# Kernel optimization log

Hardware: AMD Instinct MI355X
Metric: run time of the kernel (lower is better)

The kernel has to match this reference:

```python
import jax, jax.numpy as jnp
import numpy as np
from jax.ops import segment_sum, segment_max

N_NODES = 10000
N_EDGES = 160000
N_GRAPHS = 32
IN_DIM = 128
HID = 256
HEADS = 4


def setup_inputs() -> dict:
    key = jax.random.key(0)
    ks = jax.random.split(key, 12)
    x = jax.random.normal(ks[0], (N_NODES, IN_DIM), dtype=jnp.float32)
    edge_index = jax.random.randint(ks[1], (2, N_EDGES), 0, N_NODES, dtype=jnp.int64)
    batch = jnp.sort(jax.random.randint(ks[2], (N_NODES,), 0, N_GRAPHS, dtype=jnp.int64))
    s = 0.05
    params = {
        "W1": jax.random.normal(ks[3], (IN_DIM, HID), dtype=jnp.float32) * s,
        "b1": jnp.zeros((HID,), dtype=jnp.float32),
        "W2": jax.random.normal(ks[4], (HID, HID), dtype=jnp.float32) * s,
        "b2": jnp.zeros((HID,), dtype=jnp.float32),
        "Wg": jax.random.normal(ks[5], (HID, HEADS * HID), dtype=jnp.float32) * s,
        "att_src": jax.random.normal(ks[6], (HEADS, HID), dtype=jnp.float32) * s,
        "att_dst": jax.random.normal(ks[7], (HEADS, HID), dtype=jnp.float32) * s,
        "bg": jnp.zeros((HID,), dtype=jnp.float32),
        "W_heads": jax.random.normal(ks[8], (HID, 4), dtype=jnp.float32) * s,
        "b_heads": jnp.zeros((4,), dtype=jnp.float32),
    }
    return {"x": x, "edge_index": edge_index, "batch": batch, **params}


def _add_self_loops(edge_index, n):
    loop = jnp.arange(n, dtype=edge_index.dtype)
    src = jnp.concatenate([edge_index[0], loop])
    dst = jnp.concatenate([edge_index[1], loop])
    return src, dst


def _gcn_conv(x, W, b, src, dst, n):
    # PyG GCNConv: add self-loops, symmetric normalization D^-1/2 A D^-1/2
    h = x @ W                                   # [N, out]
    deg = segment_sum(jnp.ones_like(src, dtype=h.dtype), dst, num_segments=n)
    dinv = jax.lax.rsqrt(jnp.maximum(deg, 1e-12))
    coef = dinv[src] * dinv[dst]                # [E+N]
    out = segment_sum(h[src] * coef[:, None], dst, num_segments=n)
    return out + b


def _gat_conv(x, Wg, att_src, att_dst, bg, src, dst, n):
    # PyG GATConv(heads=4, concat=False): mean over heads, leaky_relu slope 0.2
    h = (x @ Wg).reshape(n, HEADS, HID)         # [N, H, C]
    a_src = jnp.einsum('nhc,hc->nh', h, att_src)
    a_dst = jnp.einsum('nhc,hc->nh', h, att_dst)
    e = jax.nn.leaky_relu(a_src[src] + a_dst[dst], 0.2)   # [E+N, H]
    m = segment_max(e, dst, num_segments=n)
    e = jnp.exp(e - m[dst])
    z = segment_sum(e, dst, num_segments=n)
    alpha = e / (z[dst] + 1e-16)                # softmax over edges into each dst
    out = segment_sum(h[src] * alpha[:, :, None], dst, num_segments=n)  # [N, H, C]
    return out.mean(axis=1) + bg


def reference(x, edge_index, batch, W1, b1, W2, b2, Wg, att_src, att_dst, bg, W_heads, b_heads):
    n = x.shape[0]
    src, dst = _add_self_loops(edge_index, n)
    h1 = jax.nn.relu(_gcn_conv(x, W1, b1, src, dst, n))
    h2 = jax.nn.relu(_gcn_conv(h1, W2, b2, src, dst, n))
    h3 = jax.nn.relu(_gat_conv(h2, Wg, att_src, att_dst, bg, src, dst, n))
    # global_mean_pool
    ones = jnp.ones((n,), dtype=h3.dtype)
    cnt = segment_sum(ones, batch, num_segments=N_GRAPHS)
    pooled = segment_sum(h3, batch, num_segments=N_GRAPHS) / jnp.maximum(cnt, 1.0)[:, None]
    # four scalar heads stacked: cols = [energy_absorption, elastic_modulus, ballistic_limit, penetration_resistance]
    return pooled @ W_heads + b_heads           # [G, 4]
```

## Files before the change

### kernel.cpp

```cpp
#include <hip/hip_runtime.h>
#include <cmath>

#define IN_DIM 128
#define HID 256
#define NHEADS 4
#define NGRAPHS 32

typedef unsigned short u16;
typedef __attribute__((ext_vector_type(8))) short bfrag8;
typedef __attribute__((ext_vector_type(4))) float f32x4;

__device__ __forceinline__ u16 f2bf(float x) {
  unsigned u = __float_as_uint(x);
  unsigned r = (u + 0x7fffu + ((u >> 16) & 1u)) >> 16;
  return (u16)r;
}
__device__ __forceinline__ float bf2f(u16 v) {
  return __uint_as_float(((unsigned)v) << 16);
}

__global__ __launch_bounds__(256) void count_edges_k(const int* __restrict__ dst,
                                                     int* __restrict__ cnt, int E) {
  int i = blockIdx.x * 256 + threadIdx.x;
  if (i < E) atomicAdd(&cnt[dst[i]], 1);
}

__global__ __launch_bounds__(1024) void scan_k(const int* __restrict__ cnt,
                                               int* __restrict__ row_ptr,
                                               float* __restrict__ dinv, int n) {
  __shared__ int sdata[1024];
  __shared__ int s_carry;
  if (threadIdx.x == 0) s_carry = 0;
  __syncthreads();
  int nchunks = (n + 1023) >> 10;
  for (int c = 0; c < nchunks; c++) {
    int i = (c << 10) + threadIdx.x;
    int v = (i < n) ? cnt[i] : 0;
    sdata[threadIdx.x] = v;
    __syncthreads();
    for (int off = 1; off < 1024; off <<= 1) {
      int t = (threadIdx.x >= off) ? sdata[threadIdx.x - off] : 0;
      __syncthreads();
      sdata[threadIdx.x] += t;
      __syncthreads();
    }
    int excl = sdata[threadIdx.x] - v;
    if (i < n) {
      row_ptr[i] = s_carry + excl;
      dinv[i] = rsqrtf((float)(v + 1));
    }
    __syncthreads();
    if (threadIdx.x == 0) s_carry += sdata[1023];
    __syncthreads();
  }
  if (threadIdx.x == 0) row_ptr[n] = s_carry;
}

__global__ __launch_bounds__(256) void fill_csr_k(const int* __restrict__ src,
                                                  const int* __restrict__ dst,
                                                  const int* __restrict__ row_ptr,
                                                  int* __restrict__ cursor,
                                                  int* __restrict__ csr_src, int E) {
  int i = blockIdx.x * 256 + threadIdx.x;
  if (i < E) {
    int d = dst[i];
    int p = atomicAdd(&cursor[d], 1);
    csr_src[row_ptr[d] + p] = src[i];
  }
}

__global__ __launch_bounds__(256) void pack_a_k(const float* __restrict__ A,
                                                u16* __restrict__ Ap,
                                                int K, int KT, int nfrag) {
  int wid = blockIdx.x * 4 + (threadIdx.x >> 6);
  int lane = threadIdx.x & 63;
  if (wid >= nfrag * KT) return;
  int fm = wid / KT, kt = wid - fm * KT;
  int m = fm * 16 + (lane & 15);
  int kb = kt * 32 + (lane >> 4) * 8;
  const float* src = A + (size_t)m * K + kb;
  float4 v0 = *(const float4*)src;
  float4 v1 = *(const float4*)(src + 4);
  float vv[8] = {v0.x, v0.y, v0.z, v0.w, v1.x, v1.y, v1.z, v1.w};
  u16 hi[8], lo[8];
  #pragma unroll
  for (int j = 0; j < 8; j++) {
    u16 h = f2bf(vv[j]);
    hi[j] = h;
    lo[j] = f2bf(vv[j] - bf2f(h));
  }
  u16* dst = Ap + ((size_t)fm * KT + kt) * 1024 + lane * 8;
  *(ushort4*)(dst)       = make_ushort4(hi[0], hi[1], hi[2], hi[3]);
  *(ushort4*)(dst + 4)   = make_ushort4(hi[4], hi[5], hi[6], hi[7]);
  *(ushort4*)(dst + 512) = make_ushort4(lo[0], lo[1], lo[2], lo[3]);
  *(ushort4*)(dst + 516) = make_ushort4(lo[4], lo[5], lo[6], lo[7]);
}

__global__ __launch_bounds__(256) void pack_b_k(const float* __restrict__ B,
                                                u16* __restrict__ Bp,
                                                int N, int KT, int nfrag) {
  int wid = blockIdx.x * 4 + (threadIdx.x >> 6);
  int lane = threadIdx.x & 63;
  if (wid >= nfrag * KT) return;
  int fn = wid / KT, kt = wid - fn * KT;
  int n = fn * 16 + (lane & 15);
  int kb = kt * 32 + (lane >> 4) * 8;
  float vv[8];
  #pragma unroll
  for (int j = 0; j < 8; j++) vv[j] = B[(size_t)(kb + j) * N + n];
  u16 hi[8], lo[8];
  #pragma unroll
  for (int j = 0; j < 8; j++) {
    u16 h = f2bf(vv[j]);
    hi[j] = h;
    lo[j] = f2bf(vv[j] - bf2f(h));
  }
  u16* dst = Bp + ((size_t)fn * KT + kt) * 1024 + lane * 8;
  *(ushort4*)(dst)       = make_ushort4(hi[0], hi[1], hi[2], hi[3]);
  *(ushort4*)(dst + 4)   = make_ushort4(hi[4], hi[5], hi[6], hi[7]);
  *(ushort4*)(dst + 512) = make_ushort4(lo[0], lo[1], lo[2], lo[3]);
  *(ushort4*)(dst + 516) = make_ushort4(lo[4], lo[5], lo[6], lo[7]);
}

template <int KT, int OMODE, bool ALO>
__global__ __launch_bounds__(256) void mfma_gemm_k(const u16* __restrict__ Ap,
                                                   const u16* __restrict__ Bp,
                                                   u16* __restrict__ Cb,
                                                   int M, int Nn) {
  int tid = threadIdx.x;
  int w = tid >> 6, lane = tid & 63;
  int wm = w >> 1, wn = w & 1;
  int fm0 = blockIdx.y * 4 + wm * 2;
  int fn0 = blockIdx.x * 4 + wn * 2;
  f32x4 acc[2][2] = {};
  #pragma unroll
  for (int kt = 0; kt < KT; kt++) {
    bfrag8 a_hi[2], a_lo[2], b_hi[2], b_lo[2];
    #pragma unroll
    for (int f = 0; f < 2; f++) {
      const u16* pa = Ap + ((size_t)(fm0 + f) * KT + kt) * 1024 + lane * 8;
      a_hi[f] = *(const bfrag8*)pa;
      if constexpr (ALO) a_lo[f] = *(const bfrag8*)(pa + 512);
      const u16* pb = Bp + ((size_t)(fn0 + f) * KT + kt) * 1024 + lane * 8;
      b_hi[f] = *(const bfrag8*)pb;
      b_lo[f] = *(const bfrag8*)(pb + 512);
    }
    #pragma unroll
    for (int f = 0; f < 2; f++) {
      #pragma unroll
      for (int g = 0; g < 2; g++) {
        acc[f][g] = __builtin_amdgcn_mfma_f32_16x16x32_bf16(a_hi[f], b_hi[g], acc[f][g], 0, 0, 0);
        acc[f][g] = __builtin_amdgcn_mfma_f32_16x16x32_bf16(a_hi[f], b_lo[g], acc[f][g], 0, 0, 0);
        if constexpr (ALO)
          acc[f][g] = __builtin_amdgcn_mfma_f32_16x16x32_bf16(a_lo[f], b_hi[g], acc[f][g], 0, 0, 0);
      }
    }
  }
  int r0 = (lane >> 4) * 4;
  int cl = lane & 15;
  #pragma unroll
  for (int f = 0; f < 2; f++) {
    #pragma unroll
    for (int g = 0; g < 2; g++) {
      int col = (fn0 + g) * 16 + cl;
      #pragma unroll
      for (int r = 0; r < 4; r++) {
        int row = (fm0 + f) * 16 + r0 + r;
        if (row < M) {
          if constexpr (OMODE == 1) {
            int head = col >> 8, cc = col & 255;
            Cb[((size_t)head * Nn + row) * HID + cc] = f2bf(acc[f][g][r]);
          } else {
            Cb[(size_t)row * HID + col] = f2bf(acc[f][g][r]);
          }
        }
      }
    }
  }
}

template <bool LOGITS, bool PACK_LO>
__global__ __launch_bounds__(256) void gcn_agg_k(const u16* __restrict__ t,
                                                 const int* __restrict__ row_ptr,
                                                 const int* __restrict__ csr_src,
                                                 const float* __restrict__ dinv,
                                                 const float* __restrict__ bias,
                                                 u16* __restrict__ apack,
                                                 const float* __restrict__ w_s,
                                                 const float* __restrict__ w_d,
                                                 float* __restrict__ a_src,
                                                 float* __restrict__ a_dst) {
  int i = blockIdx.x;
  int tt = threadIdx.x;
  int q = tt >> 6, lane = tt & 63;
  int c4 = lane * 4;
  __shared__ float4 s_part[4][64];
  float di = dinv[i];
  int beg = row_ptr[i], end = row_ptr[i + 1];
  float4 acc = make_float4(0.f, 0.f, 0.f, 0.f);
  if (q == 0) {
    ushort4 u = *(const ushort4*)&t[(size_t)i * HID + c4];
    float w = di * di;
    acc.x = w * bf2f(u.x); acc.y = w * bf2f(u.y);
    acc.z = w * bf2f(u.z); acc.w = w * bf2f(u.w);
  }
  int e = beg + q;
  for (; e + 4 < end; e += 8) {
    int s0 = csr_src[e], s1 = csr_src[e + 4];
    float w0 = dinv[s0] * di, w1 = dinv[s1] * di;
    ushort4 u0 = *(const ushort4*)&t[(size_t)s0 * HID + c4];
    ushort4 u1 = *(const ushort4*)&t[(size_t)s1 * HID + c4];
    acc.x += w0 * bf2f(u0.x) + w1 * bf2f(u1.x);
    acc.y += w0 * bf2f(u0.y) + w1 * bf2f(u1.y);
    acc.z += w0 * bf2f(u0.z) + w1 * bf2f(u1.z);
    acc.w += w0 * bf2f(u0.w) + w1 * bf2f(u1.w);
  }
  if (e < end) {
    int s = csr_src[e];
    float w = dinv[s] * di;
    ushort4 u = *(const ushort4*)&t[(size_t)s * HID + c4];
    acc.x += w * bf2f(u.x); acc.y += w * bf2f(u.y);
    acc.z += w * bf2f(u.z); acc.w += w * bf2f(u.w);
  }
  s_part[q][lane] = acc;
  __syncthreads();
  int c = tt;
  const float* f = (const float*)s_part;
  float a = (f[c] + f[256 + c]) + (f[512 + c] + f[768 + c]);
  float v = fmaxf(a + bias[c], 0.f);
  {
    int fm = i >> 4, kt = c >> 5;
    int pl = (i & 15) + 16 * ((c >> 3) & 3);
    int j = c & 7;
    u16 h = f2bf(v);
    size_t base = ((size_t)fm * 8 + kt) * 1024 + pl * 8 + j;
    apack[base] = h;
    if constexpr (PACK_LO) apack[base + 512] = f2bf(v - bf2f(h));
  }
  if constexpr (LOGITS) {
    __shared__ float s_rs[4][NHEADS];
    __shared__ float s_rd[4][NHEADS];
    float4 wsv = *(const float4*)&w_s[c * NHEADS];
    float4 wdv = *(const float4*)&w_d[c * NHEADS];
    float ps[NHEADS] = {v * wsv.x, v * wsv.y, v * wsv.z, v * wsv.w};
    float pd[NHEADS] = {v * wdv.x, v * wdv.y, v * wdv.z, v * wdv.w};
    #pragma unroll
    for (int off = 32; off; off >>= 1) {
      #pragma unroll
      for (int h = 0; h < NHEADS; h++) {
        ps[h] += __shfl_xor(ps[h], off);
        pd[h] += __shfl_xor(pd[h], off);
      }
    }
    int wv = q;
    if (lane == 0) {
      #pragma unroll
      for (int h = 0; h < NHEADS; h++) { s_rs[wv][h] = ps[h]; s_rd[wv][h] = pd[h]; }
    }
    __syncthreads();
    if (tt < NHEADS)
      a_src[i * NHEADS + tt] = s_rs[0][tt] + s_rs[1][tt] + s_rs[2][tt] + s_rs[3][tt];
    else if (tt < 2 * NHEADS) {
      int h = tt - NHEADS;
      a_dst[i * NHEADS + h] = s_rd[0][h] + s_rd[1][h] + s_rd[2][h] + s_rd[3][h];
    }
  }
}

__global__ __launch_bounds__(256) void watt_k(const float* __restrict__ Wg,
                                              const float* __restrict__ att_src,
                                              const float* __restrict__ att_dst,
                                              float* __restrict__ w_s,
                                              float* __restrict__ w_d) {
  int k = blockIdx.x;
  int c = threadIdx.x;
  int wv = c >> 6, ln = c & 63;
  __shared__ float red_s[4][NHEADS];
  __shared__ float red_d[4][NHEADS];
  #pragma unroll
  for (int h = 0; h < NHEADS; h++) {
    float w = Wg[(size_t)k * (NHEADS * HID) + h * HID + c];
    float vs = w * att_src[h * HID + c];
    float vd = w * att_dst[h * HID + c];
    #pragma unroll
    for (int off = 32; off; off >>= 1) {
      vs += __shfl_xor(vs, off);
      vd += __shfl_xor(vd, off);
    }
    if (ln == 0) { red_s[wv][h] = vs; red_d[wv][h] = vd; }
  }
  __syncthreads();
  if (c < NHEADS) {
    w_s[k * NHEADS + c] = red_s[0][c] + red_s[1][c] + red_s[2][c] + red_s[3][c];
    w_d[k * NHEADS + c] = red_d[0][c] + red_d[1][c] + red_d[2][c] + red_d[3][c];
  }
}

__device__ __forceinline__ float lrelu02(float x) { return x > 0.f ? x : 0.2f * x; }

__global__ __launch_bounds__(256) void gat_agg_k(const u16* __restrict__ hgT,
                                                 const int* __restrict__ row_ptr,
                                                 const int* __restrict__ csr_src,
                                                 const float* __restrict__ a_src,
                                                 const float* __restrict__ a_dst,
                                                 const float* __restrict__ bg,
                                                 float* __restrict__ out, int Nn) {
  int i = blockIdx.x;
  int t = threadIdx.x;
  int hw = t >> 6, lane = t & 63;
  __shared__ int s_src[NHEADS][64];
  __shared__ float s_al[NHEADS][64];
  __shared__ float s_acc[NHEADS][64][4];
  int beg = row_ptr[i], end = row_ptr[i + 1];
  int deg = end - beg;
  float adh = a_dst[i * NHEADS + hw];
  const u16* slab = hgT + (size_t)hw * Nn * HID;
  int c4 = lane * 4;
  float a0 = 0.f, a1 = 0.f, a2 = 0.f, a3 = 0.f;

  if (deg <= 63) {
    int s = (lane < deg) ? csr_src[beg + lane] : i;
    bool valid = (lane <= deg);
    float logit = valid ? lrelu02(a_src[s * NHEADS + hw] + adh) : -INFINITY;
    float m = logit;
    #pragma unroll
    for (int off = 32; off; off >>= 1) m = fmaxf(m, __shfl_xor(m, off));
    float ex = valid ? expf(logit - m) : 0.f;
    float z = ex;
    #pragma unroll
    for (int off = 32; off; off >>= 1) z += __shfl_xor(z, off);
    float al = ex / (z + 1e-16f);
    s_src[hw][lane] = s;
    s_al[hw][lane] = al;
    int nk = deg + 1;
    int e = 0;
    for (; e + 3 < nk; e += 4) {
      int s0 = s_src[hw][e + 0], s1 = s_src[hw][e + 1];
      int s2 = s_src[hw][e + 2], s3 = s_src[hw][e + 3];
      float w0 = s_al[hw][e + 0], w1 = s_al[hw][e + 1];
      float w2 = s_al[hw][e + 2], w3 = s_al[hw][e + 3];
      ushort4 v0 = *(const ushort4*)&slab[(size_t)s0 * HID + c4];
      ushort4 v1 = *(const ushort4*)&slab[(size_t)s1 * HID + c4];
      ushort4 v2 = *(const ushort4*)&slab[(size_t)s2 * HID + c4];
      ushort4 v3 = *(const ushort4*)&slab[(size_t)s3 * HID + c4];
      a0 += w0 * bf2f(v0.x) + w1 * bf2f(v1.x) + w2 * bf2f(v2.x) + w3 * bf2f(v3.x);
      a1 += w0 * bf2f(v0.y) + w1 * bf2f(v1.y) + w2 * bf2f(v2.y) + w3 * bf2f(v3.y);
      a2 += w0 * bf2f(v0.z) + w1 * bf2f(v1.z) + w2 * bf2f(v2.z) + w3 * bf2f(v3.z);
      a3 += w0 * bf2f(v0.w) + w1 * bf2f(v1.w) + w2 * bf2f(v2.w) + w3 * bf2f(v3.w);
    }
    for (; e < nk; e++) {
      int se = s_src[hw][e];
      float ae = s_al[hw][e];
      ushort4 v = *(const ushort4*)&slab[(size_t)se * HID + c4];
      a0 += ae * bf2f(v.x); a1 += ae * bf2f(v.y);
      a2 += ae * bf2f(v.z); a3 += ae * bf2f(v.w);
    }
  } else {
    float lself = lrelu02(a_src[i * NHEADS + hw] + adh);
    float m = lself;
    for (int e = beg + lane; e < end; e += 64)
      m = fmaxf(m, lrelu02(a_src[csr_src[e] * NHEADS + hw] + adh));
    #pragma unroll
    for (int off = 32; off; off >>= 1) m = fmaxf(m, __shfl_xor(m, off));
    float z = (lane == 0) ? expf(lself - m) : 0.f;
    for (int e = beg + lane; e < end; e += 64)
      z += expf(lrelu02(a_src[csr_src[e] * NHEADS + hw] + adh) - m);
    #pragma unroll
    for (int off = 32; off; off >>= 1) z += __shfl_xor(z, off);
    float iz = 1.f / (z + 1e-16f);
    {
      float ae = expf(lself - m) * iz;
      ushort4 v = *(const ushort4*)&slab[(size_t)i * HID + c4];
      a0 += ae * bf2f(v.x); a1 += ae * bf2f(v.y);
      a2 += ae * bf2f(v.z); a3 += ae * bf2f(v.w);
    }
    for (int base = beg; base < end; base += 64) {
      int mc = min(64, end - base);
      int s = (lane < mc) ? csr_src[base + lane] : 0;
      float al = (lane < mc)
                     ? expf(lrelu02(a_src[s * NHEADS + hw] + adh) - m) * iz
                     : 0.f;
      s_src[hw][lane] = s;
      s_al[hw][lane] = al;
      for (int e = 0; e < mc; e++) {
        int se = s_src[hw][e];
        float ae = s_al[hw][e];
        ushort4 v = *(const ushort4*)&slab[(size_t)se * HID + c4];
        a0 += ae * bf2f(v.x); a1 += ae * bf2f(v.y);
        a2 += ae * bf2f(v.z); a3 += ae * bf2f(v.w);
      }
    }
  }
  s_acc[hw][lane][0] = a0;
  s_acc[hw][lane][1] = a1;
  s_acc[hw][lane][2] = a2;
  s_acc[hw][lane][3] = a3;
  __syncthreads();
  int c = t;
  const float* f = (const float*)s_acc;
  float a = (f[c] + f[256 + c]) + (f[512 + c] + f[768 + c]);
  out[(size_t)i * HID + c] = fmaxf(a * 0.25f + bg[c], 0.f);
}

#define POOL_CHUNK 50
__global__ __launch_bounds__(256) void pool_acc_k(const float* __restrict__ h3,
                                                  const int* __restrict__ batch,
                                                  float* __restrict__ pooled,
                                                  float* __restrict__ gcnt, int N) {
  int c = threadIdx.x;
  int i0 = blockIdx.x * POOL_CHUNK;
  int i1 = min(i0 + POOL_CHUNK, N);
  if (i0 >= N) return;
  float acc = 0.f;
  int cur = batch[i0];
  int cnt_local = 0;
  for (int i = i0; i < i1; i++) {
    int g = batch[i];
    if (g != cur) {
      atomicAdd(&pooled[cur * HID + c], acc);
      if (c == 0) atomicAdd(&gcnt[cur], (float)cnt_local);
      acc = 0.f;
      cnt_local = 0;
      cur = g;
    }
    acc += h3[(size_t)i * HID + c];
    cnt_local++;
  }
  atomicAdd(&pooled[cur * HID + c], acc);
  if (c == 0) atomicAdd(&gcnt[cur], (float)cnt_local);
}

__global__ __launch_bounds__(128) void head_k(const float* __restrict__ pooled,
                                              const float* __restrict__ gcnt,
                                              const float* __restrict__ W_heads,
                                              const float* __restrict__ b_heads,
                                              float* __restrict__ out) {
  int tid = threadIdx.x;
  if (tid >= NGRAPHS * 4) return;
  int g = tid >> 2, k = tid & 3;
  float invc = 1.f / fmaxf(gcnt[g], 1.f);
  float acc = 0.f;
  for (int c = 0; c < HID; c++) acc += pooled[g * HID + c] * W_heads[c * 4 + k];
  out[g * 4 + k] = acc * invc + b_heads[k];
}

extern "C" void kernel_launch(void* const* d_in, const int* in_sizes, int n_in,
                              void* d_out, int out_size, void* d_ws, size_t ws_size,
                              hipStream_t stream) {
  const float* x = (const float*)d_in[0];
  const int* ei = (const int*)d_in[1];
  const int* batch = (const int*)d_in[2];
  const float* W1 = (const float*)d_in[3];
  const float* b1 = (const float*)d_in[4];
  const float* W2 = (const float*)d_in[5];
  const float* b2 = (const float*)d_in[6];
  const float* Wg = (const float*)d_in[7];
  const float* att_src = (const float*)d_in[8];
  const float* att_dst = (const float*)d_in[9];
  const float* bg = (const float*)d_in[10];
  const float* W_heads = (const float*)d_in[11];
  const float* b_heads = (const float*)d_in[12];
  float* out = (float*)d_out;

  const int N = in_sizes[0] / IN_DIM;
  const int E = in_sizes[1] / 2;
  const int* src = ei;
  const int* dst = ei + E;

  const int NFM = N / 16;
  const int NFMP = ((N + 63) / 64) * 4;

  char* ws = (char*)d_ws;
  size_t off = 0;
  auto take = [&](size_t bytes) -> char* {
    char* p = ws + off;
    off = (off + bytes + 255) & ~(size_t)255;
    return p;
  };
  int* cnt      = (int*)take((size_t)N * 4);
  int* row_ptr  = (int*)take((size_t)(N + 1) * 4);
  int* cursor   = (int*)take((size_t)N * 4);
  int* csr_src  = (int*)take((size_t)E * 4);
  float* dinv   = (float*)take((size_t)N * 4);
  float* a_srcv = (float*)take((size_t)N * NHEADS * 4);
  float* a_dstv = (float*)take((size_t)N * NHEADS * 4);
  float* w_s    = (float*)take((size_t)HID * NHEADS * 4);
  float* w_d    = (float*)take((size_t)HID * NHEADS * 4);
  float* pooled = (float*)take((size_t)NGRAPHS * HID * 4 + NGRAPHS * 4);
  float* gcnt   = pooled + NGRAPHS * HID;
  u16*   tb     = (u16*)take((size_t)N * HID * 2);
  float* h3     = (float*)take((size_t)N * HID * 4);
  u16*   hgT    = (u16*)take((size_t)N * NHEADS * HID * 2);
  u16*   xp     = (u16*)take((size_t)NFMP * 4 * 1024 * 2);
  u16*   h1p    = (u16*)take((size_t)NFMP * 8 * 1024 * 2);
  u16*   h2p    = (u16*)take((size_t)NFMP * 8 * 1024 * 2);
  u16*   w1p    = (u16*)take((size_t)16 * 4 * 1024 * 2);
  u16*   w2p    = (u16*)take((size_t)16 * 8 * 1024 * 2);
  u16*   wgp    = (u16*)take((size_t)64 * 8 * 1024 * 2);

  hipMemsetAsync(cnt, 0, (size_t)N * 4, stream);
  hipMemsetAsync(cursor, 0, (size_t)N * 4, stream);
  hipMemsetAsync(pooled, 0, (size_t)NGRAPHS * HID * 4 + NGRAPHS * 4, stream);

  int eb = (E + 255) / 256;
  count_edges_k<<<eb, 256, 0, stream>>>(dst, cnt, E);
  scan_k<<<1, 1024, 0, stream>>>(cnt, row_ptr, dinv, N);
  fill_csr_k<<<eb, 256, 0, stream>>>(src, dst, row_ptr, cursor, csr_src, E);
  watt_k<<<HID, 256, 0, stream>>>(Wg, att_src, att_dst, w_s, w_d);

  pack_a_k<<<(NFM * 4 + 3) / 4, 256, 0, stream>>>(x, xp, IN_DIM, 4, NFM);
  pack_b_k<<<(16 * 4 + 3) / 4, 256, 0, stream>>>(W1, w1p, HID, 4, 16);
  pack_b_k<<<(16 * 8 + 3) / 4, 256, 0, stream>>>(W2, w2p, HID, 8, 16);
  pack_b_k<<<(64 * 8 + 3) / 4, 256, 0, stream>>>(Wg, wgp, NHEADS * HID, 8, 64);

  int mg64 = (N + 63) / 64;
  mfma_gemm_k<4, 0, true><<<dim3(4, mg64), 256, 0, stream>>>(xp, w1p, tb, N, N);
  gcn_agg_k<false, true><<<N, 256, 0, stream>>>(tb, row_ptr, csr_src, dinv, b1,
                                                h1p, nullptr, nullptr, nullptr, nullptr);
  mfma_gemm_k<8, 0, true><<<dim3(4, mg64), 256, 0, stream>>>(h1p, w2p, tb, N, N);
  gcn_agg_k<true, false><<<N, 256, 0, stream>>>(tb, row_ptr, csr_src, dinv, b2,
                                                h2p, w_s, w_d, a_srcv, a_dstv);
  mfma_gemm_k<8, 1, false><<<dim3(16, mg64), 256, 0, stream>>>(h2p, wgp, hgT, N, N);
  gat_agg_k<<<N, 256, 0, stream>>>(hgT, row_ptr, csr_src, a_srcv, a_dstv, bg, h3, N);
  int pb = (N + POOL_CHUNK - 1) / POOL_CHUNK;
  pool_acc_k<<<pb, 256, 0, stream>>>(h3, batch, pooled, gcnt, N);
  head_k<<<1, 128, 0, stream>>>(pooled, gcnt, W_heads, b_heads, out);
}
```

Before: 232.5 us.

## Map one wavefront per node in aggregations, fuse prep kernels, shuffle-based scan

The GCN and GAT aggregation kernels now assign one wavefront per destination node instead of a 256-thread block. Each lane handles a contiguous slice of channels, and float4 attention logits are reduced with cross-lane shuffles instead of shared-memory reductions. The GAT GEMM writes a node-major layout so each node's head rows are contiguous. Packing and attention-weight precompute are fused into one prep launch, the scan uses wave shuffles, and the three memsets collapse into one. This cuts launches, barriers and shared-memory traffic, but each wave now does more serial edge work per node.

```diff
diff --git a/kernel.cpp b/kernel.cpp
--- a/kernel.cpp
+++ b/kernel.cpp
@@ -18,6 +18,9 @@
 __device__ __forceinline__ float bf2f(u16 v) {
   return __uint_as_float(((unsigned)v) << 16);
 }
+__device__ __forceinline__ float lof(unsigned u) { return __uint_as_float(u << 16); }
+__device__ __forceinline__ float hif(unsigned u) { return __uint_as_float(u & 0xffff0000u); }
+__device__ __forceinline__ float lrelu02(float x) { return x > 0.f ? x : 0.2f * x; }
 
 __global__ __launch_bounds__(256) void count_edges_k(const int* __restrict__ dst,
                                                      int* __restrict__ cnt, int E) {
@@ -28,32 +31,44 @@
 __global__ __launch_bounds__(1024) void scan_k(const int* __restrict__ cnt,
                                                int* __restrict__ row_ptr,
                                                float* __restrict__ dinv, int n) {
-  __shared__ int sdata[1024];
-  __shared__ int s_carry;
-  if (threadIdx.x == 0) s_carry = 0;
-  __syncthreads();
-  int nchunks = (n + 1023) >> 10;
-  for (int c = 0; c < nchunks; c++) {
-    int i = (c << 10) + threadIdx.x;
+  __shared__ int s_w[16];
+  __shared__ int s_tot;
+  int tid = threadIdx.x;
+  int wv = tid >> 6, lane = tid & 63;
+  int carry = 0;
+  int nch = (n + 1023) >> 10;
+  for (int c = 0; c < nch; c++) {
+    int i = (c << 10) + tid;
     int v = (i < n) ? cnt[i] : 0;
-    sdata[threadIdx.x] = v;
+    int incl = v;
+    #pragma unroll
+    for (int off = 1; off < 64; off <<= 1) {
+      int t = __shfl_up(incl, off);
+      if (lane >= off) incl += t;
+    }
+    if (lane == 63) s_w[wv] = incl;
     __syncthreads();
-    for (int off = 1; off < 1024; off <<= 1) {
-      int t = (threadIdx.x >= off) ? sdata[threadIdx.x - off] : 0;
-      __syncthreads();
-      sdata[threadIdx.x] += t;
-      __syncthreads();
-    }
-    int excl = sdata[threadIdx.x] - v;
+    if (tid < 16) {
+      int sv = s_w[tid];
+      int si = sv;
+      #pragma unroll
+      for (int off = 1; off < 16; off <<= 1) {
+        int t = __shfl_up(si, off, 16);
+        if (tid >= off) si += t;
+      }
+      s_w[tid] = si - sv;
+      if (tid == 15) s_tot = si;
+    }
+    __syncthreads();
+    int excl = incl - v + s_w[wv] + carry;
     if (i < n) {
-      row_ptr[i] = s_carry + excl;
+      row_ptr[i] = excl;
       dinv[i] = rsqrtf((float)(v + 1));
     }
+    carry += s_tot;
     __syncthreads();
-    if (threadIdx.x == 0) s_carry += sdata[1023];
-    __syncthreads();
-  }
-  if (threadIdx.x == 0) row_ptr[n] = s_carry;
+  }
+  if (tid == 0) row_ptr[n] = carry;
 }
 
 __global__ __launch_bounds__(256) void fill_csr_k(const int* __restrict__ src,
@@ -69,12 +84,8 @@
   }
 }
 
-__global__ __launch_bounds__(256) void pack_a_k(const float* __restrict__ A,
-                                                u16* __restrict__ Ap,
-                                                int K, int KT, int nfrag) {
-  int wid = blockIdx.x * 4 + (threadIdx.x >> 6);
-  int lane = threadIdx.x & 63;
-  if (wid >= nfrag * KT) return;
+__device__ void pack_a_dev(const float* __restrict__ A, u16* __restrict__ Ap,
+                           int K, int KT, int wid, int lane) {
   int fm = wid / KT, kt = wid - fm * KT;
   int m = fm * 16 + (lane & 15);
   int kb = kt * 32 + (lane >> 4) * 8;
@@ -89,19 +100,15 @@
     hi[j] = h;
     lo[j] = f2bf(vv[j] - bf2f(h));
   }
-  u16* dst = Ap + ((size_t)fm * KT + kt) * 1024 + lane * 8;
-  *(ushort4*)(dst)       = make_ushort4(hi[0], hi[1], hi[2], hi[3]);
-  *(ushort4*)(dst + 4)   = make_ushort4(hi[4], hi[5], hi[6], hi[7]);
-  *(ushort4*)(dst + 512) = make_ushort4(lo[0], lo[1], lo[2], lo[3]);
-  *(ushort4*)(dst + 516) = make_ushort4(lo[4], lo[5], lo[6], lo[7]);
-}
-
-__global__ __launch_bounds__(256) void pack_b_k(const float* __restrict__ B,
-                                                u16* __restrict__ Bp,
-                                                int N, int KT, int nfrag) {
-  int wid = blockIdx.x * 4 + (threadIdx.x >> 6);
-  int lane = threadIdx.x & 63;
-  if (wid >= nfrag * KT) return;
+  u16* dstp = Ap + ((size_t)fm * KT + kt) * 1024 + lane * 8;
+  *(ushort4*)(dstp)       = make_ushort4(hi[0], hi[1], hi[2], hi[3]);
+  *(ushort4*)(dstp + 4)   = make_ushort4(hi[4], hi[5], hi[6], hi[7]);
+  *(ushort4*)(dstp + 512) = make_ushort4(lo[0], lo[1], lo[2], lo[3]);
+  *(ushort4*)(dstp + 516) = make_ushort4(lo[4], lo[5], lo[6], lo[7]);
+}
+
+__device__ void pack_b_dev(const float* __restrict__ B, u16* __restrict__ Bp,
+                           int N, int KT, int wid, int lane) {
   int fn = wid / KT, kt = wid - fn * KT;
   int n = fn * 16 + (lane & 15);
   int kb = kt * 32 + (lane >> 4) * 8;
@@ -115,18 +122,69 @@
     hi[j] = h;
     lo[j] = f2bf(vv[j] - bf2f(h));
   }
-  u16* dst = Bp + ((size_t)fn * KT + kt) * 1024 + lane * 8;
-  *(ushort4*)(dst)       = make_ushort4(hi[0], hi[1], hi[2], hi[3]);
-  *(ushort4*)(dst + 4)   = make_ushort4(hi[4], hi[5], hi[6], hi[7]);
-  *(ushort4*)(dst + 512) = make_ushort4(lo[0], lo[1], lo[2], lo[3]);
-  *(ushort4*)(dst + 516) = make_ushort4(lo[4], lo[5], lo[6], lo[7]);
-}
-
-template <int KT, int OMODE, bool ALO>
+  u16* dstp = Bp + ((size_t)fn * KT + kt) * 1024 + lane * 8;
+  *(ushort4*)(dstp)       = make_ushort4(hi[0], hi[1], hi[2], hi[3]);
+  *(ushort4*)(dstp + 4)   = make_ushort4(hi[4], hi[5], hi[6], hi[7]);
+  *(ushort4*)(dstp + 512) = make_ushort4(lo[0], lo[1], lo[2], lo[3]);
+  *(ushort4*)(dstp + 516) = make_ushort4(lo[4], lo[5], lo[6], lo[7]);
+}
+
+__global__ __launch_bounds__(256) void prep_k(const float* __restrict__ x,
+                                              const float* __restrict__ W1,
+                                              const float* __restrict__ W2,
+                                              const float* __restrict__ Wg,
+                                              const float* __restrict__ att_src,
+                                              const float* __restrict__ att_dst,
+                                              u16* __restrict__ xp,
+                                              u16* __restrict__ w1p,
+                                              u16* __restrict__ w2p,
+                                              u16* __restrict__ wgp,
+                                              float* __restrict__ w_s,
+                                              float* __restrict__ w_d, int NFM) {
+  __shared__ float red_s[4][NHEADS];
+  __shared__ float red_d[4][NHEADS];
+  int b = blockIdx.x;
+  int tid = threadIdx.x;
+  int lane = tid & 63;
+  int XB = NFM;
+  if (b < XB) {
+    int wid = b * 4 + (tid >> 6);
+    if (wid < NFM * 4) pack_a_dev(x, xp, IN_DIM, 4, wid, lane);
+  } else if (b < XB + 16) {
+    pack_b_dev(W1, w1p, HID, 4, (b - XB) * 4 + (tid >> 6), lane);
+  } else if (b < XB + 48) {
+    pack_b_dev(W2, w2p, HID, 8, (b - XB - 16) * 4 + (tid >> 6), lane);
+  } else if (b < XB + 176) {
+    pack_b_dev(Wg, wgp, NHEADS * HID, 8, (b - XB - 48) * 4 + (tid >> 6), lane);
+  } else {
+    int k = b - (XB + 176);
+    int c = tid, wvv = c >> 6, ln = c & 63;
+    #pragma unroll
+    for (int h = 0; h < NHEADS; h++) {
+      float w = Wg[(size_t)k * (NHEADS * HID) + h * HID + c];
+      float vs = w * att_src[h * HID + c];
+      float vd = w * att_dst[h * HID + c];
+      #pragma unroll
+      for (int off = 32; off; off >>= 1) {
+        vs += __shfl_xor(vs, off);
+        vd += __shfl_xor(vd, off);
+      }
+      if (ln == 0) { red_s[wvv][h] = vs; red_d[wvv][h] = vd; }
+    }
+    __syncthreads();
+    if (c < NHEADS)
+      w_s[k * NHEADS + c] = red_s[0][c] + red_s[1][c] + red_s[2][c] + red_s[3][c];
+    else if (c < 2 * NHEADS) {
+      int h = c - NHEADS;
+      w_d[k * NHEADS + h] = red_d[0][h] + red_d[1][h] + red_d[2][h] + red_d[3][h];
+    }
+  }
+}
+
+template <int KT, int LDC, bool ALO>
 __global__ __launch_bounds__(256) void mfma_gemm_k(const u16* __restrict__ Ap,
                                                    const u16* __restrict__ Bp,
-                                                   u16* __restrict__ Cb,
-                                                   int M, int Nn) {
+                                                   u16* __restrict__ Cb, int M) {
   int tid = threadIdx.x;
   int w = tid >> 6, lane = tid & 63;
   int wm = w >> 1, wn = w & 1;
@@ -166,14 +224,7 @@
       #pragma unroll
       for (int r = 0; r < 4; r++) {
         int row = (fm0 + f) * 16 + r0 + r;
-        if (row < M) {
-          if constexpr (OMODE == 1) {
-            int head = col >> 8, cc = col & 255;
-            Cb[((size_t)head * Nn + row) * HID + cc] = f2bf(acc[f][g][r]);
-          } else {
-            Cb[(size_t)row * HID + col] = f2bf(acc[f][g][r]);
-          }
-        }
+        if (row < M) Cb[(size_t)row * LDC + col] = f2bf(acc[f][g][r]);
       }
     }
   }
@@ -188,218 +239,235 @@
                                                  u16* __restrict__ apack,
                                                  const float* __restrict__ w_s,
                                                  const float* __restrict__ w_d,
-                                                 float* __restrict__ a_src,
-                                                 float* __restrict__ a_dst) {
-  int i = blockIdx.x;
-  int tt = threadIdx.x;
-  int q = tt >> 6, lane = tt & 63;
+                                                 float4* __restrict__ a_src4,
+                                                 float4* __restrict__ a_dst4, int N) {
+  int wv = threadIdx.x >> 6, lane = threadIdx.x & 63;
+  int i = blockIdx.x * 4 + wv;
+  if (i >= N) return;
+  float di = dinv[i];
   int c4 = lane * 4;
-  __shared__ float4 s_part[4][64];
-  float di = dinv[i];
   int beg = row_ptr[i], end = row_ptr[i + 1];
-  float4 acc = make_float4(0.f, 0.f, 0.f, 0.f);
-  if (q == 0) {
-    ushort4 u = *(const ushort4*)&t[(size_t)i * HID + c4];
+  float a0, a1, a2, a3;
+  {
+    uint2 u = *(const uint2*)&t[(size_t)i * HID + c4];
     float w = di * di;
-    acc.x = w * bf2f(u.x); acc.y = w * bf2f(u.y);
-    acc.z = w * bf2f(u.z); acc.w = w * bf2f(u.w);
-  }
-  int e = beg + q;
-  for (; e + 4 < end; e += 8) {
-    int s0 = csr_src[e], s1 = csr_src[e + 4];
+    a0 = w * lof(u.x); a1 = w * hif(u.x); a2 = w * lof(u.y); a3 = w * hif(u.y);
+  }
+  int e = beg;
+  for (; e + 3 < end; e += 4) {
+    int s0 = csr_src[e + 0], s1 = csr_src[e + 1];
+    int s2 = csr_src[e + 2], s3 = csr_src[e + 3];
     float w0 = dinv[s0] * di, w1 = dinv[s1] * di;
-    ushort4 u0 = *(const ushort4*)&t[(size_t)s0 * HID + c4];
-    ushort4 u1 = *(const ushort4*)&t[(size_t)s1 * HID + c4];
-    acc.x += w0 * bf2f(u0.x) + w1 * bf2f(u1.x);
-    acc.y += w0 * bf2f(u0.y) + w1 * bf2f(u1.y);
-    acc.z += w0 * bf2f(u0.z) + w1 * bf2f(u1.z);
-    acc.w += w0 * bf2f(u0.w) + w1 * bf2f(u1.w);
-  }
-  if (e < end) {
+    float w2 = dinv[s2] * di, w3 = dinv[s3] * di;
+    uint2 u0 = *(const uint2*)&t[(size_t)s0 * HID + c4];
+    uint2 u1 = *(const uint2*)&t[(size_t)s1 * HID + c4];
+    uint2 u2 = *(const uint2*)&t[(size_t)s2 * HID + c4];
+    uint2 u3 = *(const uint2*)&t[(size_t)s3 * HID + c4];
+    a0 += w0 * lof(u0.x) + w1 * lof(u1.x) + w2 * lof(u2.x) + w3 * lof(u3.x);
+    a1 += w0 * hif(u0.x) + w1 * hif(u1.x) + w2 * hif(u2.x) + w3 * hif(u3.x);
+    a2 += w0 * lof(u0.y) + w1 * lof(u1.y) + w2 * lof(u2.y) + w3 * lof(u3.y);
+    a3 += w0 * hif(u0.y) + w1 * hif(u1.y) + w2 * hif(u2.y) + w3 * hif(u3.y);
+  }
+  for (; e < end; e++) {
     int s = csr_src[e];
     float w = dinv[s] * di;
-    ushort4 u = *(const ushort4*)&t[(size_t)s * HID + c4];
-    acc.x += w * bf2f(u.x); acc.y += w * bf2f(u.y);
-    acc.z += w * bf2f(u.z); acc.w += w * bf2f(u.w);
-  }
-  s_part[q][lane] = acc;
-  __syncthreads();
-  int c = tt;
-  const float* f = (const float*)s_part;
-  float a = (f[c] + f[256 + c]) + (f[512 + c] + f[768 + c]);
-  float v = fmaxf(a + bias[c], 0.f);
+    uint2 u = *(const uint2*)&t[(size_t)s * HID + c4];
+    a0 += w * lof(u.x); a1 += w * hif(u.x); a2 += w * lof(u.y); a3 += w * hif(u.y);
+  }
+  float4 bv = *(const float4*)&bias[c4];
+  float v0 = fmaxf(a0 + bv.x, 0.f), v1 = fmaxf(a1 + bv.y, 0.f);
+  float v2 = fmaxf(a2 + bv.z, 0.f), v3 = fmaxf(a3 + bv.w, 0.f);
   {
-    int fm = i >> 4, kt = c >> 5;
-    int pl = (i & 15) + 16 * ((c >> 3) & 3);
-    int j = c & 7;
-    u16 h = f2bf(v);
-    size_t base = ((size_t)fm * 8 + kt) * 1024 + pl * 8 + j;
-    apack[base] = h;
-    if constexpr (PACK_LO) apack[base + 512] = f2bf(v - bf2f(h));
+    int fm = i >> 4, kt = c4 >> 5;
+    int pl = (i & 15) + 16 * ((c4 >> 3) & 3);
+    int j0 = c4 & 7;
+    size_t base = ((size_t)fm * 8 + kt) * 1024 + pl * 8 + j0;
+    u16 h0 = f2bf(v0), h1 = f2bf(v1), h2 = f2bf(v2), h3 = f2bf(v3);
+    *(ushort4*)&apack[base] = make_ushort4(h0, h1, h2, h3);
+    if constexpr (PACK_LO)
+      *(ushort4*)&apack[base + 512] =
+          make_ushort4(f2bf(v0 - bf2f(h0)), f2bf(v1 - bf2f(h1)),
+                       f2bf(v2 - bf2f(h2)), f2bf(v3 - bf2f(h3)));
   }
   if constexpr (LOGITS) {
-    __shared__ float s_rs[4][NHEADS];
-    __shared__ float s_rd[4][NHEADS];
-    float4 wsv = *(const float4*)&w_s[c * NHEADS];
-    float4 wdv = *(const float4*)&w_d[c * NHEADS];
-    float ps[NHEADS] = {v * wsv.x, v * wsv.y, v * wsv.z, v * wsv.w};
-    float pd[NHEADS] = {v * wdv.x, v * wdv.y, v * wdv.z, v * wdv.w};
+    const float4* ws4 = (const float4*)w_s;
+    const float4* wd4 = (const float4*)w_d;
+    float4 s0 = ws4[c4 + 0], s1 = ws4[c4 + 1], s2 = ws4[c4 + 2], s3 = ws4[c4 + 3];
+    float4 d0 = wd4[c4 + 0], d1 = wd4[c4 + 1], d2 = wd4[c4 + 2], d3 = wd4[c4 + 3];
+    float ps0 = v0 * s0.x + v1 * s1.x + v2 * s2.x + v3 * s3.x;
+    float ps1 = v0 * s0.y + v1 * s1.y + v2 * s2.y + v3 * s3.y;
+    float ps2 = v0 * s0.z + v1 * s1.z + v2 * s2.z + v3 * s3.z;
+    float ps3 = v0 * s0.w + v1 * s1.w + v2 * s2.w + v3 * s3.w;
+    float pd0 = v0 * d0.x + v1 * d1.x + v2 * d2.x + v3 * d3.x;
+    float pd1 = v0 * d0.y + v1 * d1.y + v2 * d2.y + v3 * d3.y;
+    float pd2 = v0 * d0.z + v1 * d1.z + v2 * d2.z + v3 * d3.z;
+    float pd3 = v0 * d0.w + v1 * d1.w + v2 * d2.w + v3 * d3.w;
     #pragma unroll
     for (int off = 32; off; off >>= 1) {
-      #pragma unroll
-      for (int h = 0; h < NHEADS; h++) {
-        ps[h] += __shfl_xor(ps[h], off);
-        pd[h] += __shfl_xor(pd[h], off);
-      }
-    }
-    int wv = q;
+      ps0 += __shfl_xor(ps0, off); ps1 += __shfl_xor(ps1, off);
+      ps2 += __shfl_xor(ps2, off); ps3 += __shfl_xor(ps3, off);
+      pd0 += __shfl_xor(pd0, off); pd1 += __shfl_xor(pd1, off);
+      pd2 += __shfl_xor(pd2, off); pd3 += __shfl_xor(pd3, off);
+    }
     if (lane == 0) {
-      #pragma unroll
-      for (int h = 0; h < NHEADS; h++) { s_rs[wv][h] = ps[h]; s_rd[wv][h] = pd[h]; }
-    }
-    __syncthreads();
-    if (tt < NHEADS)
-      a_src[i * NHEADS + tt] = s_rs[0][tt] + s_rs[1][tt] + s_rs[2][tt] + s_rs[3][tt];
-    else if (tt < 2 * NHEADS) {
-      int h = tt - NHEADS;
-      a_dst[i * NHEADS + h] = s_rd[0][h] + s_rd[1][h] + s_rd[2][h] + s_rd[3][h];
-    }
-  }
-}
-
-__global__ __launch_bounds__(256) void watt_k(const float* __restrict__ Wg,
-                                              const float* __restrict__ att_src,
-                                              const float* __restrict__ att_dst,
-                                              float* __restrict__ w_s,
-                                              float* __restrict__ w_d) {
-  int k = blockIdx.x;
-  int c = threadIdx.x;
-  int wv = c >> 6, ln = c & 63;
-  __shared__ float red_s[4][NHEADS];
-  __shared__ float red_d[4][NHEADS];
-  #pragma unroll
-  for (int h = 0; h < NHEADS; h++) {
-    float w = Wg[(size_t)k * (NHEADS * HID) + h * HID + c];
-    float vs = w * att_src[h * HID + c];
-    float vd = w * att_dst[h * HID + c];
-    #pragma unroll
-    for (int off = 32; off; off >>= 1) {
-      vs += __shfl_xor(vs, off);
-      vd += __shfl_xor(vd, off);
-    }
-    if (ln == 0) { red_s[wv][h] = vs; red_d[wv][h] = vd; }
-  }
-  __syncthreads();
-  if (c < NHEADS) {
-    w_s[k * NHEADS + c] = red_s[0][c] + red_s[1][c] + red_s[2][c] + red_s[3][c];
-    w_d[k * NHEADS + c] = red_d[0][c] + red_d[1][c] + red_d[2][c] + red_d[3][c];
-  }
-}
-
-__device__ __forceinline__ float lrelu02(float x) { return x > 0.f ? x : 0.2f * x; }
+      a_src4[i] = make_float4(ps0, ps1, ps2, ps3);
+      a_dst4[i] = make_float4(pd0, pd1, pd2, pd3);
+    }
+  }
+}
+
+#define ACC8(U, AW, O)                                         \
+  acc[O + 0] += (AW) * lof((U).x); acc[O + 1] += (AW) * hif((U).x); \
+  acc[O + 2] += (AW) * lof((U).y); acc[O + 3] += (AW) * hif((U).y); \
+  acc[O + 4] += (AW) * lof((U).z); acc[O + 5] += (AW) * hif((U).z); \
+  acc[O + 6] += (AW) * lof((U).w); acc[O + 7] += (AW) * hif((U).w);
 
 __global__ __launch_bounds__(256) void gat_agg_k(const u16* __restrict__ hgT,
                                                  const int* __restrict__ row_ptr,
                                                  const int* __restrict__ csr_src,
-                                                 const float* __restrict__ a_src,
-                                                 const float* __restrict__ a_dst,
+                                                 const float4* __restrict__ a_src4,
+                                                 const float4* __restrict__ a_dst4,
                                                  const float* __restrict__ bg,
-                                                 float* __restrict__ out, int Nn) {
-  int i = blockIdx.x;
-  int t = threadIdx.x;
-  int hw = t >> 6, lane = t & 63;
-  __shared__ int s_src[NHEADS][64];
-  __shared__ float s_al[NHEADS][64];
-  __shared__ float s_acc[NHEADS][64][4];
+                                                 float* __restrict__ out, int N) {
+  __shared__ int s_src[4][64];
+  __shared__ float s_al[4][NHEADS][65];
+  int wv = threadIdx.x >> 6, lane = threadIdx.x & 63;
+  int i = blockIdx.x * 4 + wv;
+  if (i >= N) return;
   int beg = row_ptr[i], end = row_ptr[i + 1];
   int deg = end - beg;
-  float adh = a_dst[i * NHEADS + hw];
-  const u16* slab = hgT + (size_t)hw * Nn * HID;
-  int c4 = lane * 4;
-  float a0 = 0.f, a1 = 0.f, a2 = 0.f, a3 = 0.f;
-
+  float4 ad = a_dst4[i];
+  int hw = lane >> 4;
+  float acc[16];
+  #pragma unroll
+  for (int j = 0; j < 16; j++) acc[j] = 0.f;
+  const u16* rowbase = hgT + (size_t)lane * 16;
+
+  int nk;
   if (deg <= 63) {
     int s = (lane < deg) ? csr_src[beg + lane] : i;
     bool valid = (lane <= deg);
-    float logit = valid ? lrelu02(a_src[s * NHEADS + hw] + adh) : -INFINITY;
-    float m = logit;
-    #pragma unroll
-    for (int off = 32; off; off >>= 1) m = fmaxf(m, __shfl_xor(m, off));
-    float ex = valid ? expf(logit - m) : 0.f;
-    float z = ex;
-    #pragma unroll
-    for (int off = 32; off; off >>= 1) z += __shfl_xor(z, off);
-    float al = ex / (z + 1e-16f);
-    s_src[hw][lane] = s;
-    s_al[hw][lane] = al;
-    int nk = deg + 1;
+    float4 as = a_src4[s];
+    float l0 = valid ? lrelu02(as.x + ad.x) : -INFINITY;
+    float l1 = valid ? lrelu02(as.y + ad.y) : -INFINITY;
+    float l2 = valid ? lrelu02(as.z + ad.z) : -INFINITY;
+    float l3 = valid ? lrelu02(as.w + ad.w) : -INFINITY;
+    float m0 = l0, m1 = l1, m2 = l2, m3 = l3;
+    #pragma unroll
+    for (int off = 32; off; off >>= 1) {
+      m0 = fmaxf(m0, __shfl_xor(m0, off)); m1 = fmaxf(m1, __shfl_xor(m1, off));
+      m2 = fmaxf(m2, __shfl_xor(m2, off)); m3 = fmaxf(m3, __shfl_xor(m3, off));
+    }
+    float e0 = valid ? expf(l0 - m0) : 0.f;
+    float e1 = valid ? expf(l1 - m1) : 0.f;
+    float e2 = valid ? expf(l2 - m2) : 0.f;
+    float e3 = valid ? expf(l3 - m3) : 0.f;
+    float z0 = e0, z1 = e1, z2 = e2, z3 = e3;
+    #pragma unroll
+    for (int off = 32; off; off >>= 1) {
+      z0 += __shfl_xor(z0, off); z1 += __shfl_xor(z1, off);
+      z2 += __shfl_xor(z2, off); z3 += __shfl_xor(z3, off);
+    }
+    s_src[wv][lane] = s;
+    s_al[wv][0][lane] = e0 / (z0 + 1e-16f);
+    s_al[wv][1][lane] = e1 / (z1 + 1e-16f);
+    s_al[wv][2][lane] = e2 / (z2 + 1e-16f);
+    s_al[wv][3][lane] = e3 / (z3 + 1e-16f);
+    nk = deg + 1;
     int e = 0;
-    for (; e + 3 < nk; e += 4) {
-      int s0 = s_src[hw][e + 0], s1 = s_src[hw][e + 1];
-      int s2 = s_src[hw][e + 2], s3 = s_src[hw][e + 3];
-      float w0 = s_al[hw][e + 0], w1 = s_al[hw][e + 1];
-      float w2 = s_al[hw][e + 2], w3 = s_al[hw][e + 3];
-      ushort4 v0 = *(const ushort4*)&slab[(size_t)s0 * HID + c4];
-      ushort4 v1 = *(const ushort4*)&slab[(size_t)s1 * HID + c4];
-      ushort4 v2 = *(const ushort4*)&slab[(size_t)s2 * HID + c4];
-      ushort4 v3 = *(const ushort4*)&slab[(size_t)s3 * HID + c4];
-      a0 += w0 * bf2f(v0.x) + w1 * bf2f(v1.x) + w2 * bf2f(v2.x) + w3 * bf2f(v3.x);
-      a1 += w0 * bf2f(v0.y) + w1 * bf2f(v1.y) + w2 * bf2f(v2.y) + w3 * bf2f(v3.y);
-      a2 += w0 * bf2f(v0.z) + w1 * bf2f(v1.z) + w2 * bf2f(v2.z) + w3 * bf2f(v3.z);
-      a3 += w0 * bf2f(v0.w) + w1 * bf2f(v1.w) + w2 * bf2f(v2.w) + w3 * bf2f(v3.w);
-    }
-    for (; e < nk; e++) {
-      int se = s_src[hw][e];
-      float ae = s_al[hw][e];
-      ushort4 v = *(const ushort4*)&slab[(size_t)se * HID + c4];
-      a0 += ae * bf2f(v.x); a1 += ae * bf2f(v.y);
-      a2 += ae * bf2f(v.z); a3 += ae * bf2f(v.w);
+    for (; e + 1 < nk; e += 2) {
+      int sa = s_src[wv][e], sb = s_src[wv][e + 1];
+      float awa = s_al[wv][hw][e], awb = s_al[wv][hw][e + 1];
+      const uint4* ra = (const uint4*)(rowbase + (size_t)sa * 1024);
+      const uint4* rb = (const uint4*)(rowbase + (size_t)sb * 1024);
+      uint4 ua0 = ra[0], ua1 = ra[1];
+      uint4 ub0 = rb[0], ub1 = rb[1];
+      ACC8(ua0, awa, 0); ACC8(ua1, awa, 8);
+      ACC8(ub0, awb, 0); ACC8(ub1, awb, 8);
+    }
+    if (e < nk) {
+      int sa = s_src[wv][e];
+      float awa = s_al[wv][hw][e];
+      const uint4* ra = (const uint4*)(rowbase + (size_t)sa * 1024);
+      uint4 ua0 = ra[0], ua1 = ra[1];
+      ACC8(ua0, awa, 0); ACC8(ua1, awa, 8);
     }
   } else {
-    float lself = lrelu02(a_src[i * NHEADS + hw] + adh);
-    float m = lself;
-    for (int e = beg + lane; e < end; e += 64)
-      m = fmaxf(m, lrelu02(a_src[csr_src[e] * NHEADS + hw] + adh));
-    #pragma unroll
-    for (int off = 32; off; off >>= 1) m = fmaxf(m, __shfl_xor(m, off));
-    float z = (lane == 0) ? expf(lself - m) : 0.f;
-    for (int e = beg + lane; e < end; e += 64)
-      z += expf(lrelu02(a_src[csr_src[e] * NHEADS + hw] + adh) - m);
-    #pragma unroll
-    for (int off = 32; off; off >>= 1) z += __shfl_xor(z, off);
-    float iz = 1.f / (z + 1e-16f);
+    float4 asi = a_src4[i];
+    float ls0 = lrelu02(asi.x + ad.x), ls1 = lrelu02(asi.y + ad.y);
+    float ls2 = lrelu02(asi.z + ad.z), ls3 = lrelu02(asi.w + ad.w);
+    float m0 = ls0, m1 = ls1, m2 = ls2, m3 = ls3;
+    for (int e = beg + lane; e < end; e += 64) {
+      float4 as = a_src4[csr_src[e]];
+      m0 = fmaxf(m0, lrelu02(as.x + ad.x)); m1 = fmaxf(m1, lrelu02(as.y + ad.y));
+      m2 = fmaxf(m2, lrelu02(as.z + ad.z)); m3 = fmaxf(m3, lrelu02(as.w + ad.w));
+    }
+    #pragma unroll
+    for (int off = 32; off; off >>= 1) {
+      m0 = fmaxf(m0, __shfl_xor(m0, off)); m1 = fmaxf(m1, __shfl_xor(m1, off));
+      m2 = fmaxf(m2, __shfl_xor(m2, off)); m3 = fmaxf(m3, __shfl_xor(m3, off));
+    }
+    float z0 = (lane == 0) ? expf(ls0 - m0) : 0.f;
+    float z1 = (lane == 0) ? expf(ls1 - m1) : 0.f;
+    float z2 = (lane == 0) ? expf(ls2 - m2) : 0.f;
+    float z3 = (lane == 0) ? expf(ls3 - m3) : 0.f;
+    for (int e = beg + lane; e < end; e += 64) {
+      float4 as = a_src4[csr_src[e]];
+      z0 += expf(lrelu02(as.x + ad.x) - m0); z1 += expf(lrelu02(as.y + ad.y) - m1);
+      z2 += expf(lrelu02(as.z + ad.z) - m2); z3 += expf(lrelu02(as.w + ad.w) - m3);
+    }
+    #pragma unroll
+    for (int off = 32; off; off >>= 1) {
+      z0 += __shfl_xor(z0, off); z1 += __shfl_xor(z1, off);
+      z2 += __shfl_xor(z2, off); z3 += __shfl_xor(z3, off);
+    }
+    float iz0 = 1.f / (z0 + 1e-16f), iz1 = 1.f / (z1 + 1e-16f);
+    float iz2 = 1.f / (z2 + 1e-16f), iz3 = 1.f / (z3 + 1e-16f);
     {
-      float ae = expf(lself - m) * iz;
-      ushort4 v = *(const ushort4*)&slab[(size_t)i * HID + c4];
-      a0 += ae * bf2f(v.x); a1 += ae * bf2f(v.y);
-      a2 += ae * bf2f(v.z); a3 += ae * bf2f(v.w);
+      float w0 = expf(ls0 - m0) * iz0, w1 = expf(ls1 - m1) * iz1;
+      float w2 = expf(ls2 - m2) * iz2, w3 = expf(ls3 - m3) * iz3;
+      float aw = hw == 0 ? w0 : hw == 1 ? w1 : hw == 2 ? w2 : w3;
+      const uint4* r = (const uint4*)(rowbase + (size_t)i * 1024);
+      uint4 u0 = r[0], u1 = r[1];
+      ACC8(u0, aw, 0); ACC8(u1, aw, 8);
     }
     for (int base = beg; base < end; base += 64) {
       int mc = min(64, end - base);
-      int s = (lane < mc) ? csr_src[base + lane] : 0;
-      float al = (lane < mc)
-                     ? expf(lrelu02(a_src[s * NHEADS + hw] + adh) - m) * iz
-                     : 0.f;
-      s_src[hw][lane] = s;
-      s_al[hw][lane] = al;
+      if (lane < mc) {
+        int s = csr_src[base + lane];
+        float4 as = a_src4[s];
+        s_src[wv][lane] = s;
+        s_al[wv][0][lane] = expf(lrelu02(as.x + ad.x) - m0) * iz0;
+        s_al[wv][1][lane] = expf(lrelu02(as.y + ad.y) - m1) * iz1;
+        s_al[wv][2][lane] = expf(lrelu02(as.z + ad.z) - m2) * iz2;
+        s_al[wv][3][lane] = expf(lrelu02(as.w + ad.w) - m3) * iz3;
+      }
       for (int e = 0; e < mc; e++) {
-        int se = s_src[hw][e];
-        float ae = s_al[hw][e];
-        ushort4 v = *(const ushort4*)&slab[(size_t)se * HID + c4];
-        a0 += ae * bf2f(v.x); a1 += ae * bf2f(v.y);
-        a2 += ae * bf2f(v.z); a3 += ae * bf2f(v.w);
+        int sa = s_src[wv][e];
+        float awa = s_al[wv][hw][e];
+        const uint4* ra = (const uint4*)(rowbase + (size_t)sa * 1024);
+        uint4 ua0 = ra[0], ua1 = ra[1];
+        ACC8(ua0, awa, 0); ACC8(ua1, awa, 8);
       }
     }
   }
-  s_acc[hw][lane][0] = a0;
-  s_acc[hw][lane][1] = a1;
-  s_acc[hw][lane][2] = a2;
-  s_acc[hw][lane][3] = a3;
-  __syncthreads();
-  int c = t;
-  const float* f = (const float*)s_acc;
-  float a = (f[c] + f[256 + c]) + (f[512 + c] + f[768 + c]);
-  out[(size_t)i * HID + c] = fmaxf(a * 0.25f + bg[c], 0.f);
+  #pragma unroll
+  for (int j = 0; j < 16; j++) {
+    acc[j] += __shfl_xor(acc[j], 16);
+    acc[j] += __shfl_xor(acc[j], 32);
+  }
+  if (lane < 16) {
+    int cb = lane * 16;
+    float o[16];
+    #pragma unroll
+    for (int j = 0; j < 16; j++)
+      o[j] = fmaxf(acc[j] * 0.25f + bg[cb + j], 0.f);
+    float* op = out + (size_t)i * HID + cb;
+    *(float4*)(op + 0)  = make_float4(o[0], o[1], o[2], o[3]);
+    *(float4*)(op + 4)  = make_float4(o[4], o[5], o[6], o[7]);
+    *(float4*)(op + 8)  = make_float4(o[8], o[9], o[10], o[11]);
+    *(float4*)(op + 12) = make_float4(o[12], o[13], o[14], o[15]);
+  }
 }
 
 #define POOL_CHUNK 50
@@ -478,16 +546,17 @@
     return p;
   };
   int* cnt      = (int*)take((size_t)N * 4);
+  int* cursor   = (int*)take((size_t)N * 4);
+  float* pooled = (float*)take((size_t)NGRAPHS * HID * 4 + NGRAPHS * 4);
+  float* gcnt   = pooled + NGRAPHS * HID;
+  size_t zero_span = off;
   int* row_ptr  = (int*)take((size_t)(N + 1) * 4);
-  int* cursor   = (int*)take((size_t)N * 4);
   int* csr_src  = (int*)take((size_t)E * 4);
   float* dinv   = (float*)take((size_t)N * 4);
-  float* a_srcv = (float*)take((size_t)N * NHEADS * 4);
-  float* a_dstv = (float*)take((size_t)N * NHEADS * 4);
+  float4* a_src4 = (float4*)take((size_t)N * 16);
+  float4* a_dst4 = (float4*)take((size_t)N * 16);
   float* w_s    = (float*)take((size_t)HID * NHEADS * 4);
   float* w_d    = (float*)take((size_t)HID * NHEADS * 4);
-  float* pooled = (float*)take((size_t)NGRAPHS * HID * 4 + NGRAPHS * 4);
-  float* gcnt   = pooled + NGRAPHS * HID;
   u16*   tb     = (u16*)take((size_t)N * HID * 2);
   float* h3     = (float*)take((size_t)N * HID * 4);
   u16*   hgT    = (u16*)take((size_t)N * NHEADS * HID * 2);
@@ -498,30 +567,25 @@
   u16*   w2p    = (u16*)take((size_t)16 * 8 * 1024 * 2);
   u16*   wgp    = (u16*)take((size_t)64 * 8 * 1024 * 2);
 
-  hipMemsetAsync(cnt, 0, (size_t)N * 4, stream);
-  hipMemsetAsync(cursor, 0, (size_t)N * 4, stream);
-  hipMemsetAsync(pooled, 0, (size_t)NGRAPHS * HID * 4 + NGRAPHS * 4, stream);
+  hipMemsetAsync(cnt, 0, zero_span, stream);
 
   int eb = (E + 255) / 256;
   count_edges_k<<<eb, 256, 0, stream>>>(dst, cnt, E);
   scan_k<<<1, 1024, 0, stream>>>(cnt, row_ptr, dinv, N);
   fill_csr_k<<<eb, 256, 0, stream>>>(src, dst, row_ptr, cursor, csr_src, E);
-  watt_k<<<HID, 256, 0, stream>>>(Wg, att_src, att_dst, w_s, w_d);
-
-  pack_a_k<<<(NFM * 4 + 3) / 4, 256, 0, stream>>>(x, xp, IN_DIM, 4, NFM);
-  pack_b_k<<<(16 * 4 + 3) / 4, 256, 0, stream>>>(W1, w1p, HID, 4, 16);
-  pack_b_k<<<(16 * 8 + 3) / 4, 256, 0, stream>>>(W2, w2p, HID, 8, 16);
-  pack_b_k<<<(64 * 8 + 3) / 4, 256, 0, stream>>>(Wg, wgp, NHEADS * HID, 8, 64);
+  prep_k<<<NFM + 176 + 256, 256, 0, stream>>>(x, W1, W2, Wg, att_src, att_dst,
+                                              xp, w1p, w2p, wgp, w_s, w_d, NFM);
 
   int mg64 = (N + 63) / 64;
-  mfma_gemm_k<4, 0, true><<<dim3(4, mg64), 256, 0, stream>>>(xp, w1p, tb, N, N);
-  gcn_agg_k<false, true><<<N, 256, 0, stream>>>(tb, row_ptr, csr_src, dinv, b1,
-                                                h1p, nullptr, nullptr, nullptr, nullptr);
-  mfma_gemm_k<8, 0, true><<<dim3(4, mg64), 256, 0, stream>>>(h1p, w2p, tb, N, N);
-  gcn_agg_k<true, false><<<N, 256, 0, stream>>>(tb, row_ptr, csr_src, dinv, b2,
-                                                h2p, w_s, w_d, a_srcv, a_dstv);
-  mfma_gemm_k<8, 1, false><<<dim3(16, mg64), 256, 0, stream>>>(h2p, wgp, hgT, N, N);
-  gat_agg_k<<<N, 256, 0, stream>>>(hgT, row_ptr, csr_src, a_srcv, a_dstv, bg, h3, N);
+  int ng4 = (N + 3) / 4;
+  mfma_gemm_k<4, HID, true><<<dim3(4, mg64), 256, 0, stream>>>(xp, w1p, tb, N);
+  gcn_agg_k<false, true><<<ng4, 256, 0, stream>>>(tb, row_ptr, csr_src, dinv, b1,
+                                                  h1p, nullptr, nullptr, nullptr, nullptr, N);
+  mfma_gemm_k<8, HID, true><<<dim3(4, mg64), 256, 0, stream>>>(h1p, w2p, tb, N);
+  gcn_agg_k<true, false><<<ng4, 256, 0, stream>>>(tb, row_ptr, csr_src, dinv, b2,
+                                                  h2p, w_s, w_d, a_src4, a_dst4, N);
+  mfma_gemm_k<8, NHEADS * HID, false><<<dim3(16, mg64), 256, 0, stream>>>(h2p, wgp, hgT, N);
+  gat_agg_k<<<ng4, 256, 0, stream>>>(hgT, row_ptr, csr_src, a_src4, a_dst4, bg, h3, N);
   int pb = (N + POOL_CHUNK - 1) / POOL_CHUNK;
   pool_acc_k<<<pb, 256, 0, stream>>>(h3, batch, pooled, gcnt, N);
   head_k<<<1, 128, 0, stream>>>(pooled, gcnt, W_heads, b_heads, out);
```

New measurement: 197.2 us. -15.2%, faster.
